# Kernel optimization log

Measured on AMD Instinct MI355X. Metric: run time of the kernel, lower is better.

Reference implementation:

```python
import jax, jax.numpy as jnp
import numpy as np

NUM_HEADS = 6
TAU = 1.0


def _split_heads(y, h):
    b, n, c = y.shape
    return y.reshape(b, n, h, c // h).transpose(0, 2, 1, 3)  # b h n d


def setup_inputs() -> dict:
    key = jax.random.key(0)
    B, M, C = 8, 1026, 384
    names = ["Wq1", "Wq2", "Wk1", "Wk2", "Wv1", "Wv2", "Wo"]
    ks = jax.random.split(key, len(names) + 3)
    inp = {"x": jax.random.normal(ks[0], (B, M, C), jnp.float32)}
    for i, nm in enumerate(names):
        inp[nm] = jax.random.normal(ks[i + 1], (C, C), jnp.float32) * 0.02
        inp["b" + nm[1:]] = jnp.zeros((C,), jnp.float32)
    inp["weights"] = jax.random.normal(ks[-2], (4,), jnp.float32)
    u = jax.random.uniform(ks[-1], (4,), jnp.float32, 1e-6, 1.0 - 1e-6)
    inp["gumbel_noise"] = -jnp.log(-jnp.log(u))  # fixed gumbel sample for determinism
    return inp


def reference(x, Wq1, bq1, Wq2, bq2, Wk1, bk1, Wk2, bk2,
              Wv1, bv1, Wv2, bv2, Wo, bo, weights, gumbel_noise):
    B, M, C = x.shape
    N1 = (M - 2) // 2 + 1  # N + 1, quadrant size
    h = NUM_HEADS
    d = C // h
    scale = d ** -0.5
    x1, x2 = x[:, :N1], x[:, N1:]
    q = jnp.concatenate([_split_heads(x1 @ Wq1 + bq1, h),
                         _split_heads(x2 @ Wq2 + bq2, h)], axis=2)  # b h M d
    k = jnp.concatenate([_split_heads(x1 @ Wk1 + bk1, h),
                         _split_heads(x2 @ Wk2 + bk2, h)], axis=2)
    v1 = _split_heads(x1 @ Wv1 + bv1, h)  # b h N1 d
    v2 = _split_heads(x2 @ Wv2 + bv2, h)
    attn = jnp.einsum('bhqd,bhkd->bhqk', q, k) * scale  # b h M M
    b1 = jax.nn.softmax(attn[:, :, :N1, :N1], axis=-1)
    b2 = jax.nn.softmax(attn[:, :, :N1, N1:], axis=-1)
    b3 = jax.nn.softmax(attn[:, :, N1:, :N1], axis=-1)
    b4 = jax.nn.softmax(attn[:, :, N1:, N1:], axis=-1)
    # hard gumbel-softmax gate (straight-through)
    y_soft = jax.nn.softmax((weights + gumbel_noise) / TAU)
    y_hard = jax.nn.one_hot(jnp.argmax(y_soft), 4, dtype=y_soft.dtype)
    w = y_hard + y_soft - jax.lax.stop_gradient(y_soft)
    A = w[0] * b1 + w[1] * b2 + w[2] * b3 + w[3] * b4  # b h N1 N1
    out1 = jnp.einsum('bhqk,bhkd->bhqd', A, v1)
    out2 = jnp.einsum('bhqk,bhkd->bhqd', A, v2)
    out = jnp.concatenate([out1, out2], axis=2)  # b h M d
    out = out.transpose(0, 2, 1, 3).reshape(B, M, C)
    return out @ Wo + bo
```

## Files before the change

kernel.cpp:

```cpp
#include <hip/hip_runtime.h>

typedef unsigned short u16;
typedef short v8s __attribute__((ext_vector_type(8)));
typedef float v4f __attribute__((ext_vector_type(4)));

namespace {
constexpr int kC = 384;
constexpr int kN1 = 513;
constexpr int kH = 6;
constexpr int kBH = 48;
constexpr int kRows = 4104;
constexpr int kRows2 = 8208;
constexpr int kPld = 576;
}

__device__ __forceinline__ u16 f2b(float f) {
  unsigned int u = __float_as_uint(f);
  u += 0x7fffu + ((u >> 16) & 1u);
  return (u16)(u >> 16);
}

__device__ __forceinline__ int gumbel_argmax(const float* __restrict__ w,
                                             const float* __restrict__ g) {
  float v0 = w[0] + g[0], v1 = w[1] + g[1], v2 = w[2] + g[2], v3 = w[3] + g[3];
  int j = 0;
  float m = v0;
  if (v1 > m) { m = v1; j = 1; }
  if (v2 > m) { m = v2; j = 2; }
  if (v3 > m) { m = v3; j = 3; }
  return j;
}

__global__ __launch_bounds__(256) void prep_w(
    const float* __restrict__ Wq1, const float* __restrict__ Wq2,
    const float* __restrict__ Wk1, const float* __restrict__ Wk2,
    const float* __restrict__ Wv1, const float* __restrict__ Wv2,
    const float* __restrict__ Wo, const float* __restrict__ wts,
    const float* __restrict__ gum, u16* __restrict__ Wqt,
    u16* __restrict__ Wkt, u16* __restrict__ Wv1t, u16* __restrict__ Wv2t,
    u16* __restrict__ Wot) {
  __shared__ float tb[32][33];
  const int bx = blockIdx.x;
  const int z = bx / 144, rem = bx - z * 144;
  const int c0 = (rem % 12) * 32, r0 = (rem / 12) * 32;
  const int j = gumbel_argmax(wts, gum);
  const float* src;
  u16* dst;
  switch (z) {
    case 0: src = (j < 2) ? Wq1 : Wq2; dst = Wqt; break;
    case 1: src = (j == 0 || j == 2) ? Wk1 : Wk2; dst = Wkt; break;
    case 2: src = Wv1; dst = Wv1t; break;
    case 3: src = Wv2; dst = Wv2t; break;
    default: src = Wo; dst = Wot; break;
  }
  const int tx = threadIdx.x & 31, ty = threadIdx.x >> 5;
  for (int p = 0; p < 4; ++p)
    tb[ty + p * 8][tx] = src[(size_t)(r0 + ty + p * 8) * kC + c0 + tx];
  __syncthreads();
  for (int p = 0; p < 4; ++p)
    dst[(size_t)(c0 + ty + p * 8) * kC + r0 + tx] = f2b(tb[tx][ty + p * 8]);
}

__global__ __launch_bounds__(256) void qkv_mfma(
    const float* __restrict__ x, const u16* __restrict__ Wqt,
    const u16* __restrict__ Wkt, const u16* __restrict__ Wv1t,
    const u16* __restrict__ Wv2t, const float* __restrict__ bq1,
    const float* __restrict__ bq2, const float* __restrict__ bk1,
    const float* __restrict__ bk2, const float* __restrict__ bv1,
    const float* __restrict__ bv2, const float* __restrict__ wts,
    const float* __restrict__ gum, u16* __restrict__ Qb, u16* __restrict__ Kb,
    u16* __restrict__ Vt1, u16* __restrict__ Vt2) {
  const int bid = blockIdx.x;
  const int xcd = bid & 7;
  const int op = xcd >> 1;
  const int wu = (bid >> 3) * 2 + (xcd & 1);
  if (wu >= 99) return;
  const int mb33 = wu / 3, nb3 = wu - mb33 * 3;

  __shared__ __align__(16) u16 As[128][72];
  __shared__ __align__(16) u16 Bs[128][72];
  const int j = gumbel_argmax(wts, gum);
  const bool vmode = (op >= 2);
  const float* bias;
  int xoff;
  const u16* Wt;
  if (op == 0) {
    bias = (j < 2) ? bq1 : bq2; xoff = (j < 2) ? 0 : kN1; Wt = Wqt;
  } else if (op == 1) {
    const bool u1 = (j == 0 || j == 2);
    bias = u1 ? bk1 : bk2; xoff = u1 ? 0 : kN1; Wt = Wkt;
  } else if (op == 2) {
    bias = bv1; xoff = 0; Wt = Wv1t;
  } else {
    bias = bv2; xoff = kN1; Wt = Wv2t;
  }
  const int m0 = (vmode ? nb3 : mb33) * 128;
  const int n0 = (vmode ? mb33 : nb3) * 128;
  const int tid = threadIdx.x;
  const int lane = tid & 63, l16 = lane & 15, quad = lane >> 4;
  const int wv = tid >> 6, wr = wv >> 1, wc = wv & 1;
  const int sr = tid >> 2, sc = (tid & 3) * 16;

  v4f acc[4][4];
  const v4f z4 = {0.f, 0.f, 0.f, 0.f};
  for (int i = 0; i < 4; ++i)
    for (int n = 0; n < 4; ++n) acc[i][n] = z4;

  for (int k0 = 0; k0 < kC; k0 += 64) {
    for (int p = 0; p < 2; ++p) {
      const int r = p * 64 + sr;
      v8s v0 = {0, 0, 0, 0, 0, 0, 0, 0}, v1 = v0;
      if (!vmode) {
        const int t = m0 + r;
        if (t < kRows) {
          const int bb = t / kN1, mm = t - bb * kN1;
          const float* s = x + ((size_t)(bb * 1026 + xoff + mm)) * kC + k0 + sc;
          const float4 f0 = *(const float4*)s;
          const float4 f1 = *(const float4*)(s + 4);
          const float4 f2 = *(const float4*)(s + 8);
          const float4 f3 = *(const float4*)(s + 12);
          v0 = (v8s){(short)f2b(f0.x), (short)f2b(f0.y), (short)f2b(f0.z),
                     (short)f2b(f0.w), (short)f2b(f1.x), (short)f2b(f1.y),
                     (short)f2b(f1.z), (short)f2b(f1.w)};
          v1 = (v8s){(short)f2b(f2.x), (short)f2b(f2.y), (short)f2b(f2.z),
                     (short)f2b(f2.w), (short)f2b(f3.x), (short)f2b(f3.y),
                     (short)f2b(f3.z), (short)f2b(f3.w)};
        }
      } else {
        const u16* s = Wt + (size_t)(m0 + r) * kC + k0 + sc;
        v0 = *(const v8s*)s;
        v1 = *(const v8s*)(s + 8);
      }
      *(v8s*)&As[r][sc] = v0;
      *(v8s*)&As[r][sc + 8] = v1;
    }
    for (int p = 0; p < 2; ++p) {
      const int r = p * 64 + sr;
      v8s v0 = {0, 0, 0, 0, 0, 0, 0, 0}, v1 = v0;
      if (!vmode) {
        const u16* s = Wt + (size_t)(n0 + r) * kC + k0 + sc;
        v0 = *(const v8s*)s;
        v1 = *(const v8s*)(s + 8);
      } else {
        const int t = n0 + r;
        if (t < kRows) {
          const int bb = t / kN1, mm = t - bb * kN1;
          const float* s = x + ((size_t)(bb * 1026 + xoff + mm)) * kC + k0 + sc;
          const float4 f0 = *(const float4*)s;
          const float4 f1 = *(const float4*)(s + 4);
          const float4 f2 = *(const float4*)(s + 8);
          const float4 f3 = *(const float4*)(s + 12);
          v0 = (v8s){(short)f2b(f0.x), (short)f2b(f0.y), (short)f2b(f0.z),
                     (short)f2b(f0.w), (short)f2b(f1.x), (short)f2b(f1.y),
                     (short)f2b(f1.z), (short)f2b(f1.w)};
          v1 = (v8s){(short)f2b(f2.x), (short)f2b(f2.y), (short)f2b(f2.z),
                     (short)f2b(f2.w), (short)f2b(f3.x), (short)f2b(f3.y),
                     (short)f2b(f3.z), (short)f2b(f3.w)};
        }
      }
      *(v8s*)&Bs[r][sc] = v0;
      *(v8s*)&Bs[r][sc + 8] = v1;
    }
    __syncthreads();
    for (int ks = 0; ks < 2; ++ks) {
      v8s af[4], bfr[4];
      for (int i = 0; i < 4; ++i)
        af[i] = *(const v8s*)&As[wr * 64 + i * 16 + l16][ks * 32 + quad * 8];
      for (int n = 0; n < 4; ++n)
        bfr[n] = *(const v8s*)&Bs[wc * 64 + n * 16 + l16][ks * 32 + quad * 8];
      for (int i = 0; i < 4; ++i)
        for (int n = 0; n < 4; ++n)
          acc[i][n] = __builtin_amdgcn_mfma_f32_16x16x32_bf16(af[i], bfr[n],
                                                              acc[i][n], 0, 0, 0);
    }
    __syncthreads();
  }

  if (!vmode) {
    u16* outp = (op == 0) ? Qb : Kb;
    const float osc = (op == 0) ? 0.125f : 1.0f;
    float bv4[4];
    for (int nt = 0; nt < 4; ++nt) bv4[nt] = bias[n0 + wc * 64 + nt * 16 + l16];
    for (int i = 0; i < 4; ++i) {
      const int rowb = m0 + wr * 64 + i * 16 + quad * 4;
      for (int r = 0; r < 4; ++r) {
        const int row = rowb + r;
        if (row >= kRows) continue;
        for (int nt = 0; nt < 4; ++nt) {
          const int col = n0 + wc * 64 + nt * 16 + l16;
          outp[(size_t)row * kC + col] = f2b((acc[i][nt][r] + bv4[nt]) * osc);
        }
      }
    }
  } else {
    u16* Vt = (op == 2) ? Vt1 : Vt2;
    for (int nt = 0; nt < 4; ++nt) {
      const int t = n0 + wc * 64 + nt * 16 + l16;
      if (t >= kRows) continue;
      const int bb = t / kN1, mm = t - bb * kN1;
      for (int i = 0; i < 4; ++i) {
        const int colb = m0 + wr * 64 + i * 16 + quad * 4;
        for (int r = 0; r < 4; ++r) {
          const int col = colb + r;
          const int hh = col >> 6, d = col & 63;
          Vt[((size_t)(bb * kH + hh) * 64 + d) * kPld + mm] =
              f2b(acc[i][nt][r] + bias[col]);
        }
      }
    }
  }
}

__global__ __launch_bounds__(256) void attn_fused(const u16* __restrict__ Qb,
                                                  const u16* __restrict__ Kb,
                                                  const u16* __restrict__ Vt1,
                                                  const u16* __restrict__ Vt2,
                                                  u16* __restrict__ PRE) {
  __shared__ __align__(16) u16 Ks[64][72];
  __shared__ __align__(16) u16 Vs[128][72];
  __shared__ __align__(16) u16 Ps[4][16][72];
  const int bid = blockIdx.x;
  const int xcd = bid & 7;
  const int t6 = bid >> 3;
  const int bh = xcd * 6 + (t6 % 6);
  const int q0 = (t6 / 6) * 64;
  const int b = bh / kH, hh = bh - b * kH;
  const int tid = threadIdx.x;
  const int w = tid >> 6, lane = tid & 63, l16 = lane & 15, quad = lane >> 4;
  v8s aq0, aq1;
  {
    int qr = q0 + w * 16 + l16;
    if (qr > 512) qr = 512;
    const u16* qs = Qb + ((size_t)(b * kN1 + qr)) * kC + hh * 64 + quad * 8;
    aq0 = *(const v8s*)qs;
    aq1 = *(const v8s*)(qs + 32);
  }
  const int ksr = tid >> 2, ksc = (tid & 3) * 16;
  const int vd = tid >> 1, vc = (tid & 1) * 32;
  const u16* kbase = Kb + (size_t)b * kN1 * kC + hh * 64 + ksc;
  const u16* vbase = ((vd < 64) ? (Vt1 + ((size_t)bh * 64 + vd) * kPld)
                                : (Vt2 + ((size_t)bh * 64 + (vd - 64)) * kPld)) +
                     vc;
  v8s kr0, kr1, vr0, vr1, vr2, vr3;
  {
    const u16* s = kbase + (size_t)ksr * kC;
    kr0 = *(const v8s*)s;
    kr1 = *(const v8s*)(s + 8);
    vr0 = *(const v8s*)(vbase);
    vr1 = *(const v8s*)(vbase + 8);
    vr2 = *(const v8s*)(vbase + 16);
    vr3 = *(const v8s*)(vbase + 24);
  }
  float lsum[4] = {0.f, 0.f, 0.f, 0.f};
  v4f Oacc[8];
  const v4f z4 = {0.f, 0.f, 0.f, 0.f};
  for (int n = 0; n < 8; ++n) Oacc[n] = z4;

  for (int kt = 0; kt < 9; ++kt) {
    const int k0 = kt * 64;
    __syncthreads();
    *(v8s*)&Ks[ksr][ksc] = kr0;
    *(v8s*)&Ks[ksr][ksc + 8] = kr1;
    *(v8s*)&Vs[vd][vc] = vr0;
    *(v8s*)&Vs[vd][vc + 8] = vr1;
    *(v8s*)&Vs[vd][vc + 16] = vr2;
    *(v8s*)&Vs[vd][vc + 24] = vr3;
    __syncthreads();
    if (kt < 8) {
      int ki = k0 + 64 + ksr;
      if (ki > 512) ki = 512;
      const u16* s = kbase + (size_t)ki * kC;
      kr0 = *(const v8s*)s;
      kr1 = *(const v8s*)(s + 8);
      const u16* t = vbase + k0 + 64;
      vr0 = *(const v8s*)t;
      vr1 = *(const v8s*)(t + 8);
      vr2 = *(const v8s*)(t + 16);
      vr3 = *(const v8s*)(t + 24);
    }
    v4f sacc[4];
    for (int nt = 0; nt < 4; ++nt) sacc[nt] = z4;
    for (int nt = 0; nt < 4; ++nt) {
      const v8s bk0 = *(const v8s*)&Ks[nt * 16 + l16][quad * 8];
      sacc[nt] = __builtin_amdgcn_mfma_f32_16x16x32_bf16(aq0, bk0, sacc[nt], 0, 0, 0);
      const v8s bk1 = *(const v8s*)&Ks[nt * 16 + l16][32 + quad * 8];
      sacc[nt] = __builtin_amdgcn_mfma_f32_16x16x32_bf16(aq1, bk1, sacc[nt], 0, 0, 0);
    }
    for (int r = 0; r < 4; ++r) {
      float ps = 0.f;
      for (int nt = 0; nt < 4; ++nt) {
        const int col = k0 + nt * 16 + l16;
        const float p = (col < kN1) ? __expf(sacc[nt][r]) : 0.f;
        ps += p;
        Ps[w][quad * 4 + r][nt * 16 + l16] = f2b(p);
      }
      lsum[r] += ps;
    }
    for (int kc = 0; kc < 2; ++kc) {
      const v8s ap = *(const v8s*)&Ps[w][l16][kc * 32 + quad * 8];
      for (int n = 0; n < 8; ++n) {
        const v8s bv = *(const v8s*)&Vs[n * 16 + l16][kc * 32 + quad * 8];
        Oacc[n] = __builtin_amdgcn_mfma_f32_16x16x32_bf16(ap, bv, Oacc[n], 0, 0, 0);
      }
    }
  }
  float rinv[4];
  for (int r = 0; r < 4; ++r) {
    float s = lsum[r];
    for (int o = 1; o <= 8; o <<= 1) s += __shfl_xor(s, o);
    rinv[r] = 1.f / s;
  }
  for (int n = 0; n < 8; ++n) {
    const int col = hh * 64 + (n & 3) * 16 + l16;
    const int rbase = b * 1026 + ((n < 4) ? 0 : kN1);
    for (int r = 0; r < 4; ++r) {
      const int q = q0 + w * 16 + quad * 4 + r;
      if (q >= kN1) continue;
      PRE[(size_t)(rbase + q) * kC + col] = f2b(Oacc[n][r] * rinv[r]);
    }
  }
}

__global__ __launch_bounds__(256) void out_mfma(const u16* __restrict__ PRE,
                                                const u16* __restrict__ Wot,
                                                const float* __restrict__ bo,
                                                float* __restrict__ OUT) {
  __shared__ __align__(16) u16 As[128][72];
  __shared__ __align__(16) u16 Bs[128][72];
  const int m0 = blockIdx.x * 128, n0 = blockIdx.y * 128;
  const int tid = threadIdx.x;
  const int lane = tid & 63, l16 = lane & 15, quad = lane >> 4;
  const int wv = tid >> 6, wr = wv >> 1, wc = wv & 1;
  const int sr = tid >> 2, sc = (tid & 3) * 16;
  v4f acc[4][4];
  const v4f z4 = {0.f, 0.f, 0.f, 0.f};
  for (int i = 0; i < 4; ++i)
    for (int n = 0; n < 4; ++n) acc[i][n] = z4;
  for (int k0 = 0; k0 < kC; k0 += 64) {
    for (int p = 0; p < 2; ++p) {
      const int r = p * 64 + sr;
      v8s v0 = {0, 0, 0, 0, 0, 0, 0, 0}, v1 = v0;
      const int row = m0 + r;
      if (row < kRows2) {
        const u16* s = PRE + (size_t)row * kC + k0 + sc;
        v0 = *(const v8s*)s;
        v1 = *(const v8s*)(s + 8);
      }
      *(v8s*)&As[r][sc] = v0;
      *(v8s*)&As[r][sc + 8] = v1;
      const u16* s2 = Wot + (size_t)(n0 + r) * kC + k0 + sc;
      *(v8s*)&Bs[r][sc] = *(const v8s*)s2;
      *(v8s*)&Bs[r][sc + 8] = *(const v8s*)(s2 + 8);
    }
    __syncthreads();
    for (int ks = 0; ks < 2; ++ks) {
      v8s af[4], bfr[4];
      for (int i = 0; i < 4; ++i)
        af[i] = *(const v8s*)&As[wr * 64 + i * 16 + l16][ks * 32 + quad * 8];
      for (int n = 0; n < 4; ++n)
        bfr[n] = *(const v8s*)&Bs[wc * 64 + n * 16 + l16][ks * 32 + quad * 8];
      for (int i = 0; i < 4; ++i)
        for (int n = 0; n < 4; ++n)
          acc[i][n] = __builtin_amdgcn_mfma_f32_16x16x32_bf16(af[i], bfr[n],
                                                              acc[i][n], 0, 0, 0);
    }
    __syncthreads();
  }
  float bv4[4];
  for (int nt = 0; nt < 4; ++nt) bv4[nt] = bo[n0 + wc * 64 + nt * 16 + l16];
  for (int i = 0; i < 4; ++i) {
    const int rowb = m0 + wr * 64 + i * 16 + quad * 4;
    for (int r = 0; r < 4; ++r) {
      const int row = rowb + r;
      if (row >= kRows2) continue;
      for (int nt = 0; nt < 4; ++nt) {
        const int col = n0 + wc * 64 + nt * 16 + l16;
        OUT[(size_t)row * kC + col] = acc[i][nt][r] + bv4[nt];
      }
    }
  }
}

extern "C" void kernel_launch(void* const* d_in, const int* in_sizes, int n_in,
                              void* d_out, int out_size, void* d_ws,
                              size_t ws_size, hipStream_t stream) {
  const float* x = (const float*)d_in[0];
  const float* Wq1 = (const float*)d_in[1];
  const float* bq1 = (const float*)d_in[2];
  const float* Wq2 = (const float*)d_in[3];
  const float* bq2 = (const float*)d_in[4];
  const float* Wk1 = (const float*)d_in[5];
  const float* bk1 = (const float*)d_in[6];
  const float* Wk2 = (const float*)d_in[7];
  const float* bk2 = (const float*)d_in[8];
  const float* Wv1 = (const float*)d_in[9];
  const float* bv1 = (const float*)d_in[10];
  const float* Wv2 = (const float*)d_in[11];
  const float* bv2 = (const float*)d_in[12];
  const float* Wo = (const float*)d_in[13];
  const float* bo = (const float*)d_in[14];
  const float* wts = (const float*)d_in[15];
  const float* gum = (const float*)d_in[16];

  u16* Wqt = (u16*)d_ws;
  u16* Wkt = Wqt + 147456;
  u16* Wv1t = Wkt + 147456;
  u16* Wv2t = Wv1t + 147456;
  u16* Wot = Wv2t + 147456;
  u16* Qb = Wot + 147456;
  u16* Kb = Qb + (size_t)kRows * kC;
  u16* Vt1 = Kb + (size_t)kRows * kC;
  u16* Vt2 = Vt1 + (size_t)kBH * 64 * kPld;
  u16* PRE = Vt2 + (size_t)kBH * 64 * kPld;

  prep_w<<<dim3(720), 256, 0, stream>>>(Wq1, Wq2, Wk1, Wk2, Wv1, Wv2, Wo, wts,
                                        gum, Wqt, Wkt, Wv1t, Wv2t, Wot);
  qkv_mfma<<<dim3(400), 256, 0, stream>>>(
      x, Wqt, Wkt, Wv1t, Wv2t, bq1, bq2, bk1, bk2, bv1, bv2, wts, gum, Qb, Kb,
      Vt1, Vt2);
  attn_fused<<<dim3(432), 256, 0, stream>>>(Qb, Kb, Vt1, Vt2, PRE);
  out_mfma<<<dim3(65, 3), 256, 0, stream>>>(PRE, Wot, bo, (float*)d_out);
}
```

Baseline: 148.2 us.

## Share P tile across waves and split PV output columns per wave

The P·V stage changes from each wave owning 16 query rows against all 128 V columns to each wave owning 32 V columns against all 64 shared query rows. P goes into a block-wide shared tile, and row sums are exchanged through shared memory. Each wave now reuses its V fragments across four row tiles, so fewer V reads hit LDS. The column mask is specialised for the last tile, and an extra barrier per iteration is added.

```diff
diff --git a/kernel.cpp b/kernel.cpp
--- a/kernel.cpp
+++ b/kernel.cpp
@@ -218,7 +218,8 @@
                                                   u16* __restrict__ PRE) {
   __shared__ __align__(16) u16 Ks[64][72];
   __shared__ __align__(16) u16 Vs[128][72];
-  __shared__ __align__(16) u16 Ps[4][16][72];
+  __shared__ __align__(16) u16 Ps[64][72];
+  __shared__ float lsumS[64];
   const int bid = blockIdx.x;
   const int xcd = bid & 7;
   const int t6 = bid >> 3;
@@ -252,9 +253,10 @@
     vr3 = *(const v8s*)(vbase + 24);
   }
   float lsum[4] = {0.f, 0.f, 0.f, 0.f};
-  v4f Oacc[8];
+  v4f Oacc[4][2];
   const v4f z4 = {0.f, 0.f, 0.f, 0.f};
-  for (int n = 0; n < 8; ++n) Oacc[n] = z4;
+  for (int mi = 0; mi < 4; ++mi)
+    for (int ni = 0; ni < 2; ++ni) Oacc[mi][ni] = z4;
 
   for (int kt = 0; kt < 9; ++kt) {
     const int k0 = kt * 64;
@@ -286,37 +288,58 @@
       const v8s bk1 = *(const v8s*)&Ks[nt * 16 + l16][32 + quad * 8];
       sacc[nt] = __builtin_amdgcn_mfma_f32_16x16x32_bf16(aq1, bk1, sacc[nt], 0, 0, 0);
     }
-    for (int r = 0; r < 4; ++r) {
-      float ps = 0.f;
-      for (int nt = 0; nt < 4; ++nt) {
-        const int col = k0 + nt * 16 + l16;
-        const float p = (col < kN1) ? __expf(sacc[nt][r]) : 0.f;
-        ps += p;
-        Ps[w][quad * 4 + r][nt * 16 + l16] = f2b(p);
-      }
-      lsum[r] += ps;
-    }
+    if (kt < 8) {
+      for (int r = 0; r < 4; ++r) {
+        float ps = 0.f;
+        for (int nt = 0; nt < 4; ++nt) {
+          const float p = __expf(sacc[nt][r]);
+          ps += p;
+          Ps[w * 16 + quad * 4 + r][nt * 16 + l16] = f2b(p);
+        }
+        lsum[r] += ps;
+      }
+    } else {
+      for (int r = 0; r < 4; ++r) {
+        float ps = 0.f;
+        for (int nt = 0; nt < 4; ++nt) {
+          const float p =
+              (nt == 0 && l16 == 0) ? __expf(sacc[nt][r]) : 0.f;
+          ps += p;
+          Ps[w * 16 + quad * 4 + r][nt * 16 + l16] = f2b(p);
+        }
+        lsum[r] += ps;
+      }
+    }
+    __syncthreads();
     for (int kc = 0; kc < 2; ++kc) {
-      const v8s ap = *(const v8s*)&Ps[w][l16][kc * 32 + quad * 8];
-      for (int n = 0; n < 8; ++n) {
-        const v8s bv = *(const v8s*)&Vs[n * 16 + l16][kc * 32 + quad * 8];
-        Oacc[n] = __builtin_amdgcn_mfma_f32_16x16x32_bf16(ap, bv, Oacc[n], 0, 0, 0);
-      }
-    }
-  }
-  float rinv[4];
+      v8s bv[2];
+      for (int ni = 0; ni < 2; ++ni)
+        bv[ni] = *(const v8s*)&Vs[w * 32 + ni * 16 + l16][kc * 32 + quad * 8];
+      for (int mi = 0; mi < 4; ++mi) {
+        const v8s ap = *(const v8s*)&Ps[mi * 16 + l16][kc * 32 + quad * 8];
+        for (int ni = 0; ni < 2; ++ni)
+          Oacc[mi][ni] = __builtin_amdgcn_mfma_f32_16x16x32_bf16(
+              ap, bv[ni], Oacc[mi][ni], 0, 0, 0);
+      }
+    }
+  }
   for (int r = 0; r < 4; ++r) {
     float s = lsum[r];
     for (int o = 1; o <= 8; o <<= 1) s += __shfl_xor(s, o);
-    rinv[r] = 1.f / s;
-  }
-  for (int n = 0; n < 8; ++n) {
-    const int col = hh * 64 + (n & 3) * 16 + l16;
-    const int rbase = b * 1026 + ((n < 4) ? 0 : kN1);
+    if (l16 == 0) lsumS[w * 16 + quad * 4 + r] = s;
+  }
+  __syncthreads();
+  const int colb = hh * 64 + ((w * 32) & 63);
+  const int rbase = b * 1026 + ((w < 2) ? 0 : kN1);
+  for (int mi = 0; mi < 4; ++mi) {
     for (int r = 0; r < 4; ++r) {
-      const int q = q0 + w * 16 + quad * 4 + r;
+      const int q = q0 + mi * 16 + quad * 4 + r;
       if (q >= kN1) continue;
-      PRE[(size_t)(rbase + q) * kC + col] = f2b(Oacc[n][r] * rinv[r]);
+      const float rinv = 1.f / lsumS[mi * 16 + quad * 4 + r];
+      for (int ni = 0; ni < 2; ++ni) {
+        const int col = colb + ni * 16 + l16;
+        PRE[(size_t)(rbase + q) * kC + col] = f2b(Oacc[mi][ni][r] * rinv);
+      }
     }
   }
 }
```

New measurement: 148.4 us. No clear change (+0.1%).
